# Kernel tuning notes

Hardware: AMD Instinct MI355X
Metric: run time of the kernel (lower is better)

The kernel has to match this reference:

```python
import jax, jax.numpy as jnp
import numpy as np

CH = 512
CK = CH // 8  # 64

def conv1x1(w, x):
    # w: [out, in], x: [B, in, H, W] -> [B, out, H, W]
    return jnp.einsum('oc,bchw->bohw', w, x)

def maxpool2(x):
    B, C, H, W = x.shape
    return x.reshape(B, C, H // 2, 2, W // 2, 2).max(axis=(3, 5))

def setup_inputs() -> dict:
    key = jax.random.key(0)
    ks = jax.random.split(key, 5)
    B, H, W = 16, 64, 64
    x = jax.random.normal(ks[0], (B, CH, H, W), dtype=jnp.float32)
    scale = 1.0 / np.sqrt(CH)
    Wt = jax.random.normal(ks[1], (CK, CH), dtype=jnp.float32) * scale
    Wp = jax.random.normal(ks[2], (CK, CH), dtype=jnp.float32) * scale
    Wg = jax.random.normal(ks[3], (CK, CH), dtype=jnp.float32) * scale
    Wo = jax.random.normal(ks[4], (CH, CK), dtype=jnp.float32) * (1.0 / np.sqrt(CK))
    gamma = jnp.float32(0.1)  # nonzero so backward through attention path is exercised
    return {'x': x, 'Wt': Wt, 'Wp': Wp, 'Wg': Wg, 'Wo': Wo, 'gamma': gamma}

def reference(x, Wt, Wp, Wg, Wo, gamma):
    B, C, H, W = x.shape
    N = H * W          # query positions
    M = N // 4         # pooled key/value positions
    theta = conv1x1(Wt, x).reshape(B, CK, N)            # [B, ck, N]
    phi = maxpool2(conv1x1(Wp, x)).reshape(B, CK, M)    # [B, ck, M]
    g = maxpool2(conv1x1(Wg, x)).reshape(B, CK, M)      # [B, ck, M]
    scores = jnp.einsum('bcn,bcm->bnm', theta, phi)     # [B, N, M]
    beta = jax.nn.softmax(scores, axis=-1)
    o = jnp.einsum('bcm,bnm->bcn', g, beta)             # [B, ck, N]
    o = conv1x1(Wo, o.reshape(B, CK, H, W))             # [B, C, H, W]
    return gamma * o + x
```

## Files before the change

### kernel.cpp

```cpp
#include <hip/hip_runtime.h>

#define CHN 512
#define CKD 64
#define NPOS 4096
#define MPOS 1024

typedef __attribute__((ext_vector_type(8))) short bf16x8;
typedef __attribute__((ext_vector_type(4))) float f32x4;
typedef __attribute__((ext_vector_type(8))) unsigned short u16x8;

static constexpr size_t OFF_O   = 0;
static constexpr size_t OFF_THT = 4194304;
static constexpr size_t OFF_PHT = 6291456;
static constexpr size_t OFF_GB  = 6815744;
static constexpr size_t OFF_WBF = 7340032;
static constexpr size_t OFF_WOB = 7389184;

__device__ __forceinline__ unsigned short f2bf(float f) {
  union { float f; unsigned int u; } v; v.f = f;
  unsigned int r = v.u + 0x7FFFu + ((v.u >> 16) & 1u);
  return (unsigned short)(r >> 16);
}

__device__ __forceinline__ void gl2lds16(const void* g, void* l) {
  __builtin_amdgcn_global_load_lds(
      (const __attribute__((address_space(1))) unsigned int*)g,
      (__attribute__((address_space(3))) unsigned int*)l, 16, 0, 0);
}

__global__ __launch_bounds__(256) void prep_w_kernel(
    const float* __restrict__ Wt, const float* __restrict__ Wp,
    const float* __restrict__ Wg, const float* __restrict__ Wo,
    unsigned short* __restrict__ wbf, unsigned short* __restrict__ wobf)
{
  int id = blockIdx.x * 256 + threadIdx.x;
  if (id < 98304) {
    int mat = id >> 15, r = id & 32767;
    const float* W = (mat == 0) ? Wt : (mat == 1) ? Wp : Wg;
    wbf[id] = f2bf(W[r]);
  } else {
    int j = id - 98304;
    wobf[j] = f2bf(Wo[j]);
  }
}

__global__ __launch_bounds__(256) void qkv_fused_kernel(
    const float* __restrict__ x,
    const unsigned short* __restrict__ wbf,
    unsigned short* __restrict__ thT, unsigned short* __restrict__ phT,
    unsigned short* __restrict__ gbf)
{
  __shared__ unsigned short sXb[64 * 132];
  __shared__ unsigned short sW[3 * 64 * 64];

  const int bx = blockIdx.x;
  const int b  = blockIdx.y;
  const int t  = threadIdx.x;
  const int w   = t >> 6;
  const int l   = t & 63;
  const int l16 = l & 15;
  const int lhi = l >> 4;
  const int n0  = bx * 128;

  const float* xb = x + (size_t)b * CHN * NPOS + n0;

  f32x4 acc[3][2][4];
#pragma unroll
  for (int m = 0; m < 3; ++m)
#pragma unroll
    for (int nf = 0; nf < 2; ++nf)
#pragma unroll
      for (int ckf = 0; ckf < 4; ++ckf) acc[m][nf][ckf] = (f32x4){0.f, 0.f, 0.f, 0.f};

  for (int c0 = 0; c0 < CHN; c0 += 64) {
    if (c0) __syncthreads();
#pragma unroll
    for (int i = 0; i < 8; ++i) {
      int row  = i * 8 + (t >> 5);
      int col4 = t & 31;
      float4 v = *(const float4*)(xb + (size_t)(c0 + row) * NPOS + col4 * 4);
      ushort4 u;
      u.x = f2bf(v.x); u.y = f2bf(v.y); u.z = f2bf(v.z); u.w = f2bf(v.w);
      *(ushort4*)&sXb[row * 132 + col4 * 4] = u;
    }
#pragma unroll
    for (int mi = 0; mi < 6; ++mi) {
      int mat = mi >> 1;
      int row = ((mi & 1) * 4 + w) * 8 + (l >> 3);
      int sbyte = (l & 7) * 16;
      const char* g = (const char*)wbf +
          ((((size_t)mat * 64 + row) * CHN + c0) << 1) + (sbyte ^ ((row & 7) << 4));
      gl2lds16(g, (char*)sW + mi * 4096 + w * 1024);
    }
    __syncthreads();

#pragma unroll
    for (int ks = 0; ks < 2; ++ks) {
      const int cu = ks * 32 + lhi * 8;
      bf16x8 a[2];
#pragma unroll
      for (int nf = 0; nf < 2; ++nf) {
        const int rn = 16 * w + 64 * nf + l16;
        bf16x8 av;
#pragma unroll
        for (int e = 0; e < 8; ++e)
          av[e] = (short)sXb[(cu + e) * 132 + rn];
        a[nf] = av;
      }
#pragma unroll
      for (int m = 0; m < 3; ++m)
#pragma unroll
        for (int ckf = 0; ckf < 4; ++ckf) {
          int rw = ckf * 16 + l16;
          bf16x8 bb = *(const bf16x8*)&sW[m * 4096 + rw * 64 + ((ks * 32 + lhi * 8) ^ ((rw & 7) * 8))];
          acc[m][0][ckf] = __builtin_amdgcn_mfma_f32_16x16x32_bf16(a[0], bb, acc[m][0][ckf], 0, 0, 0);
          acc[m][1][ckf] = __builtin_amdgcn_mfma_f32_16x16x32_bf16(a[1], bb, acc[m][1][ckf], 0, 0, 0);
        }
    }
  }

  unsigned short* th = thT + (size_t)b * NPOS * 64;
#pragma unroll
  for (int nf = 0; nf < 2; ++nf)
#pragma unroll
    for (int r = 0; r < 4; ++r) {
      int n = n0 + 16 * w + 64 * nf + lhi * 4 + r;
#pragma unroll
      for (int ckf = 0; ckf < 4; ++ckf)
        th[(size_t)n * 64 + ckf * 16 + l16] = f2bf(acc[0][nf][ckf][r]);
    }

  unsigned short* ph = phT + (size_t)b * MPOS * 64;
  unsigned short* gb = gbf + (size_t)b * CKD * MPOS;
#pragma unroll
  for (int pr = 0; pr < 2; ++pr) {
    int mcol = bx * 32 + 8 * w + lhi * 2 + pr;
#pragma unroll
    for (int ckf = 0; ckf < 4; ++ckf) {
      int ck = ckf * 16 + l16;
      float vp = fmaxf(fmaxf(acc[1][0][ckf][2 * pr], acc[1][0][ckf][2 * pr + 1]),
                       fmaxf(acc[1][1][ckf][2 * pr], acc[1][1][ckf][2 * pr + 1]));
      float vg = fmaxf(fmaxf(acc[2][0][ckf][2 * pr], acc[2][0][ckf][2 * pr + 1]),
                       fmaxf(acc[2][1][ckf][2 * pr], acc[2][1][ckf][2 * pr + 1]));
      ph[(size_t)mcol * 64 + ck] = f2bf(vp);
      gb[(size_t)ck * MPOS + mcol] = f2bf(vg);
    }
  }
}

__global__ __launch_bounds__(256) void attn_kernel(
    const unsigned short* __restrict__ thT,
    const unsigned short* __restrict__ phT,
    const unsigned short* __restrict__ gbf,
    unsigned short* __restrict__ obf)
{
  __shared__ unsigned short sTh[64 * 64];
  __shared__ unsigned short sPhi[64 * 64];
  __shared__ unsigned short sG[64 * 64];
  __shared__ unsigned short sP[64 * 64];

  const int qt = blockIdx.x;
  const int b  = blockIdx.y;
  const int t  = threadIdx.x;
  const int w   = t >> 6;
  const int l   = t & 63;
  const int l16 = l & 15;
  const int lhi = l >> 4;

  {
    const unsigned short* src = thT + ((size_t)b * NPOS + (size_t)qt * 64) * 64;
#pragma unroll
    for (int c = t; c < 512; c += 256) {
      int row = c >> 3, c8 = c & 7;
      *(f32x4*)&sTh[row * 64 + ((c8 * 8) ^ ((row & 7) * 8))] =
          *(const f32x4*)(src + row * 64 + c8 * 8);
    }
  }

  f32x4 oacc[4];
  float m_run[4], l_run[4];
#pragma unroll
  for (int i = 0; i < 4; ++i) {
    oacc[i] = (f32x4){0.f, 0.f, 0.f, 0.f};
    m_run[i] = -1e30f; l_run[i] = 0.f;
  }

  const unsigned short* phb = phT + (size_t)b * MPOS * 64;
  const unsigned short* gb  = gbf + (size_t)b * CKD * MPOS;

  for (int mt = 0; mt < 16; ++mt) {
    __syncthreads();
#pragma unroll
    for (int c = t; c < 512; c += 256) {
      int row = c >> 3, c8 = c & 7;
      *(f32x4*)&sPhi[row * 64 + ((c8 * 8) ^ ((row & 7) * 8))] =
          *(const f32x4*)(phb + (size_t)(mt * 64 + row) * 64 + c8 * 8);
    }
#pragma unroll
    for (int c = t; c < 512; c += 256) {
      int row = c >> 3, c8 = c & 7;
      *(f32x4*)&sG[row * 64 + ((c8 * 8) ^ ((row & 7) * 8))] =
          *(const f32x4*)(gb + (size_t)row * MPOS + mt * 64 + c8 * 8);
    }
    __syncthreads();

    f32x4 sacc[4];
#pragma unroll
    for (int mf = 0; mf < 4; ++mf) sacc[mf] = (f32x4){0.f, 0.f, 0.f, 0.f};
#pragma unroll
    for (int ks = 0; ks < 2; ++ks) {
      const int q  = 16 * w + l16;
      const int ob = lhi * 8 + 32 * ks;
      bf16x8 a = *(const bf16x8*)&sTh[q * 64 + (ob ^ ((q & 7) * 8))];
#pragma unroll
      for (int mf = 0; mf < 4; ++mf) {
        const int m = l16 + 16 * mf;
        bf16x8 bb = *(const bf16x8*)&sPhi[m * 64 + (ob ^ ((m & 7) * 8))];
        sacc[mf] = __builtin_amdgcn_mfma_f32_16x16x32_bf16(a, bb, sacc[mf], 0, 0, 0);
      }
    }

    float sc[4];
#pragma unroll
    for (int r = 0; r < 4; ++r) {
      float mx = fmaxf(fmaxf(sacc[0][r], sacc[1][r]), fmaxf(sacc[2][r], sacc[3][r]));
      mx = fmaxf(mx, __shfl_xor(mx, 1, 64));
      mx = fmaxf(mx, __shfl_xor(mx, 2, 64));
      mx = fmaxf(mx, __shfl_xor(mx, 4, 64));
      mx = fmaxf(mx, __shfl_xor(mx, 8, 64));
      float mnew = fmaxf(m_run[r], mx);
      sc[r] = __expf(m_run[r] - mnew);
      m_run[r] = mnew;
      float rs = 0.f;
#pragma unroll
      for (int mf = 0; mf < 4; ++mf) {
        float p = __expf(sacc[mf][r] - mnew);
        sacc[mf][r] = p;
        rs += p;
      }
      rs += __shfl_xor(rs, 1, 64);
      rs += __shfl_xor(rs, 2, 64);
      rs += __shfl_xor(rs, 4, 64);
      rs += __shfl_xor(rs, 8, 64);
      l_run[r] = l_run[r] * sc[r] + rs;
    }

#pragma unroll
    for (int r = 0; r < 4; ++r) {
      const int qq = 16 * w + lhi * 4 + r;
      const int swz = (qq & 7) * 8;
#pragma unroll
      for (int mf = 0; mf < 4; ++mf) {
        const int m = l16 + 16 * mf;
        sP[qq * 64 + ((m & 0x38) ^ swz) + (m & 7)] = f2bf(sacc[mf][r]);
      }
    }

#pragma unroll
    for (int ckf = 0; ckf < 4; ++ckf)
#pragma unroll
      for (int r = 0; r < 4; ++r) oacc[ckf][r] *= sc[r];

#pragma unroll
    for (int ks = 0; ks < 2; ++ks) {
      const int q  = 16 * w + l16;
      const int ob = lhi * 8 + 32 * ks;
      bf16x8 a = *(const bf16x8*)&sP[q * 64 + (ob ^ ((q & 7) * 8))];
#pragma unroll
      for (int ckf = 0; ckf < 4; ++ckf) {
        const int ck = l16 + 16 * ckf;
        bf16x8 bb = *(const bf16x8*)&sG[ck * 64 + (ob ^ ((ck & 7) * 8))];
        oacc[ckf] = __builtin_amdgcn_mfma_f32_16x16x32_bf16(a, bb, oacc[ckf], 0, 0, 0);
      }
    }
  }

  float inv[4];
#pragma unroll
  for (int r = 0; r < 4; ++r) inv[r] = 1.0f / l_run[r];

  unsigned short* ob = obf + (size_t)b * NPOS * 64;
#pragma unroll
  for (int r = 0; r < 4; ++r) {
    int n = qt * 64 + 16 * w + lhi * 4 + r;
#pragma unroll
    for (int ckf = 0; ckf < 4; ++ckf)
      ob[(size_t)n * 64 + ckf * 16 + l16] = f2bf(oacc[ckf][r] * inv[r]);
  }
}

__global__ __launch_bounds__(256) void outconv_mfma_kernel(
    const float* __restrict__ x,
    const unsigned short* __restrict__ wobf,
    const unsigned short* __restrict__ obf,
    const float* __restrict__ gamma_p, float* __restrict__ outp)
{
  __shared__ unsigned short sO[256 * 64];
  __shared__ unsigned short sWo[64 * 64];

  const int nt = blockIdx.x;
  const int ct = blockIdx.y;
  const int b  = blockIdx.z;
  const int t  = threadIdx.x;
  const int w   = t >> 6;
  const int l   = t & 63;
  const int l16 = l & 15;
  const int lhi = l >> 4;

#pragma unroll
  for (int i = 0; i < 8; ++i) {
    int cidx = i * 256 + t;
    int row = cidx >> 3, sub = cidx & 7;
    const char* g = (const char*)obf +
        ((((size_t)b * NPOS + nt * 256 + row) * 64) << 1) + ((sub * 16) ^ ((row & 7) << 4));
    gl2lds16(g, (char*)sO + (i * 256 + w * 64) * 16);
  }
#pragma unroll
  for (int i = 0; i < 2; ++i) {
    int cidx = i * 256 + t;
    int row = cidx >> 3, sub = cidx & 7;
    const char* g = (const char*)wobf +
        ((((size_t)(ct * 64 + row)) * 64) << 1) + ((sub * 16) ^ ((row & 7) << 4));
    gl2lds16(g, (char*)sWo + (i * 256 + w * 64) * 16);
  }

  const float gv = *gamma_p;
  float4 xv[4][4];
#pragma unroll
  for (int nf = 0; nf < 4; ++nf) {
    const int n = nt * 256 + w * 64 + nf * 16 + lhi * 4;
#pragma unroll
    for (int cf = 0; cf < 4; ++cf) {
      const int co = ct * 64 + cf * 16 + l16;
      xv[nf][cf] = *(const float4*)(x + ((size_t)b * CHN + co) * NPOS + n);
    }
  }
  __syncthreads();

  f32x4 acc[4][4];
#pragma unroll
  for (int nf = 0; nf < 4; ++nf)
#pragma unroll
    for (int cf = 0; cf < 4; ++cf) acc[nf][cf] = (f32x4){0.f, 0.f, 0.f, 0.f};

#pragma unroll
  for (int ks = 0; ks < 2; ++ks) {
    const int cu = ks * 32 + lhi * 8;
    bf16x8 a[4];
#pragma unroll
    for (int nf = 0; nf < 4; ++nf) {
      int rn = w * 64 + nf * 16 + l16;
      a[nf] = *(const bf16x8*)&sO[rn * 64 + (cu ^ ((rn & 7) * 8))];
    }
#pragma unroll
    for (int cf = 0; cf < 4; ++cf) {
      int rw = cf * 16 + l16;
      bf16x8 bb = *(const bf16x8*)&sWo[rw * 64 + (cu ^ ((rw & 7) * 8))];
#pragma unroll
      for (int nf = 0; nf < 4; ++nf)
        acc[nf][cf] = __builtin_amdgcn_mfma_f32_16x16x32_bf16(a[nf], bb, acc[nf][cf], 0, 0, 0);
    }
  }

#pragma unroll
  for (int nf = 0; nf < 4; ++nf) {
    const int n = nt * 256 + w * 64 + nf * 16 + lhi * 4;
#pragma unroll
    for (int cf = 0; cf < 4; ++cf) {
      const int co = ct * 64 + cf * 16 + l16;
      const size_t off = ((size_t)b * CHN + co) * NPOS + n;
      float4 rr;
      rr.x = fmaf(gv, acc[nf][cf][0], xv[nf][cf].x);
      rr.y = fmaf(gv, acc[nf][cf][1], xv[nf][cf].y);
      rr.z = fmaf(gv, acc[nf][cf][2], xv[nf][cf].z);
      rr.w = fmaf(gv, acc[nf][cf][3], xv[nf][cf].w);
      *(float4*)(outp + off) = rr;
    }
  }
}

extern "C" void kernel_launch(void* const* d_in, const int* in_sizes, int n_in,
                              void* d_out, int out_size, void* d_ws, size_t ws_size,
                              hipStream_t stream)
{
  const float* x     = (const float*)d_in[0];
  const float* Wt    = (const float*)d_in[1];
  const float* Wp    = (const float*)d_in[2];
  const float* Wg    = (const float*)d_in[3];
  const float* Wo    = (const float*)d_in[4];
  const float* gamma = (const float*)d_in[5];
  float* out = (float*)d_out;
  float* ws  = (float*)d_ws;

  unsigned short* obf = (unsigned short*)(ws + OFF_O);
  unsigned short* thT = (unsigned short*)(ws + OFF_THT);
  unsigned short* phT = (unsigned short*)(ws + OFF_PHT);
  unsigned short* gbf = (unsigned short*)(ws + OFF_GB);
  unsigned short* wbf = (unsigned short*)(ws + OFF_WBF);
  unsigned short* wob = (unsigned short*)(ws + OFF_WOB);

  prep_w_kernel<<<dim3(512), 256, 0, stream>>>(Wt, Wp, Wg, Wo, wbf, wob);
  qkv_fused_kernel<<<dim3(32, 16), 256, 0, stream>>>(x, wbf, thT, phT, gbf);
  attn_kernel<<<dim3(64, 16), 256, 0, stream>>>(thT, phT, gbf, obf);
  outconv_mfma_kernel<<<dim3(16, 8, 16), 256, 0, stream>>>(x, wob, obf, gamma, out);
}
```

Before: 141.5 us.

## Double attention query tile per block and load K/V tiles via direct global-to-LDS

The attention kernel now processes 128 query rows per block (two 16-row fragments per wave) instead of 64, so each loaded phi/g tile is reused across twice as many queries and the grid halves. Tile loads switch from register-staged copies to the gl2lds16 direct global-to-LDS path with the swizzle applied on the source address. Softmax shuffles are narrowed to 16-lane width. Costs are doubled accumulator register pressure and fewer blocks (512), which may reduce occupancy and latency hiding.

```diff
diff --git a/kernel.cpp b/kernel.cpp
--- a/kernel.cpp
+++ b/kernel.cpp
@@ -154,10 +154,10 @@
     const unsigned short* __restrict__ gbf,
     unsigned short* __restrict__ obf)
 {
-  __shared__ unsigned short sTh[64 * 64];
+  __shared__ unsigned short sTh[128 * 64];
+  __shared__ unsigned short sP [128 * 64];
   __shared__ unsigned short sPhi[64 * 64];
-  __shared__ unsigned short sG[64 * 64];
-  __shared__ unsigned short sP[64 * 64];
+  __shared__ unsigned short sG [64 * 64];
 
   const int qt = blockIdx.x;
   const int b  = blockIdx.y;
@@ -168,22 +168,25 @@
   const int lhi = l >> 4;
 
   {
-    const unsigned short* src = thT + ((size_t)b * NPOS + (size_t)qt * 64) * 64;
-#pragma unroll
-    for (int c = t; c < 512; c += 256) {
-      int row = c >> 3, c8 = c & 7;
-      *(f32x4*)&sTh[row * 64 + ((c8 * 8) ^ ((row & 7) * 8))] =
-          *(const f32x4*)(src + row * 64 + c8 * 8);
-    }
-  }
-
-  f32x4 oacc[4];
-  float m_run[4], l_run[4];
-#pragma unroll
-  for (int i = 0; i < 4; ++i) {
-    oacc[i] = (f32x4){0.f, 0.f, 0.f, 0.f};
-    m_run[i] = -1e30f; l_run[i] = 0.f;
-  }
+    const char* srcb = (const char*)(thT + ((size_t)b * NPOS + (size_t)qt * 128) * 64);
+#pragma unroll
+    for (int i = 0; i < 4; ++i) {
+      int cidx = i * 256 + t;
+      int row = cidx >> 3, sub = cidx & 7;
+      gl2lds16(srcb + row * 128 + ((sub * 16) ^ ((row & 7) << 4)),
+               (char*)sTh + (i * 256 + w * 64) * 16);
+    }
+  }
+
+  f32x4 oacc[2][4];
+  float m_run[2][4], l_run[2][4];
+#pragma unroll
+  for (int qf = 0; qf < 2; ++qf)
+#pragma unroll
+    for (int i = 0; i < 4; ++i) {
+      oacc[qf][i] = (f32x4){0.f, 0.f, 0.f, 0.f};
+      m_run[qf][i] = -1e30f; l_run[qf][i] = 0.f;
+    }
 
   const unsigned short* phb = phT + (size_t)b * MPOS * 64;
   const unsigned short* gb  = gbf + (size_t)b * CKD * MPOS;
@@ -191,101 +194,113 @@
   for (int mt = 0; mt < 16; ++mt) {
     __syncthreads();
 #pragma unroll
-    for (int c = t; c < 512; c += 256) {
-      int row = c >> 3, c8 = c & 7;
-      *(f32x4*)&sPhi[row * 64 + ((c8 * 8) ^ ((row & 7) * 8))] =
-          *(const f32x4*)(phb + (size_t)(mt * 64 + row) * 64 + c8 * 8);
-    }
-#pragma unroll
-    for (int c = t; c < 512; c += 256) {
-      int row = c >> 3, c8 = c & 7;
-      *(f32x4*)&sG[row * 64 + ((c8 * 8) ^ ((row & 7) * 8))] =
-          *(const f32x4*)(gb + (size_t)row * MPOS + mt * 64 + c8 * 8);
+    for (int i = 0; i < 2; ++i) {
+      int cidx = i * 256 + t;
+      int row = cidx >> 3, sub = cidx & 7;
+      gl2lds16((const char*)(phb + (size_t)(mt * 64 + row) * 64) +
+                   ((sub * 16) ^ ((row & 7) << 4)),
+               (char*)sPhi + (i * 256 + w * 64) * 16);
+      gl2lds16((const char*)(gb + (size_t)row * MPOS + mt * 64) +
+                   ((sub * 16) ^ ((row & 7) << 4)),
+               (char*)sG + (i * 256 + w * 64) * 16);
     }
     __syncthreads();
 
-    f32x4 sacc[4];
-#pragma unroll
-    for (int mf = 0; mf < 4; ++mf) sacc[mf] = (f32x4){0.f, 0.f, 0.f, 0.f};
-#pragma unroll
-    for (int ks = 0; ks < 2; ++ks) {
-      const int q  = 16 * w + l16;
-      const int ob = lhi * 8 + 32 * ks;
-      bf16x8 a = *(const bf16x8*)&sTh[q * 64 + (ob ^ ((q & 7) * 8))];
-#pragma unroll
-      for (int mf = 0; mf < 4; ++mf) {
-        const int m = l16 + 16 * mf;
-        bf16x8 bb = *(const bf16x8*)&sPhi[m * 64 + (ob ^ ((m & 7) * 8))];
-        sacc[mf] = __builtin_amdgcn_mfma_f32_16x16x32_bf16(a, bb, sacc[mf], 0, 0, 0);
+    f32x4 sacc[2][4];
+#pragma unroll
+    for (int qf = 0; qf < 2; ++qf)
+#pragma unroll
+      for (int mf = 0; mf < 4; ++mf) sacc[qf][mf] = (f32x4){0.f, 0.f, 0.f, 0.f};
+#pragma unroll
+    for (int qf = 0; qf < 2; ++qf)
+#pragma unroll
+      for (int ks = 0; ks < 2; ++ks) {
+        const int q  = 32 * w + 16 * qf + l16;
+        const int ob = lhi * 8 + 32 * ks;
+        bf16x8 a = *(const bf16x8*)&sTh[q * 64 + (ob ^ ((q & 7) * 8))];
+#pragma unroll
+        for (int mf = 0; mf < 4; ++mf) {
+          const int m = l16 + 16 * mf;
+          bf16x8 bb = *(const bf16x8*)&sPhi[m * 64 + (ob ^ ((m & 7) * 8))];
+          sacc[qf][mf] = __builtin_amdgcn_mfma_f32_16x16x32_bf16(a, bb, sacc[qf][mf], 0, 0, 0);
+        }
       }
-    }
-
-    float sc[4];
+
+    float sc[2][4];
+#pragma unroll
+    for (int qf = 0; qf < 2; ++qf) {
+#pragma unroll
+      for (int r = 0; r < 4; ++r) {
+        float mx = fmaxf(fmaxf(sacc[qf][0][r], sacc[qf][1][r]),
+                         fmaxf(sacc[qf][2][r], sacc[qf][3][r]));
+        mx = fmaxf(mx, __shfl_xor(mx, 1, 16));
+        mx = fmaxf(mx, __shfl_xor(mx, 2, 16));
+        mx = fmaxf(mx, __shfl_xor(mx, 4, 16));
+        mx = fmaxf(mx, __shfl_xor(mx, 8, 16));
+        float mnew = fmaxf(m_run[qf][r], mx);
+        sc[qf][r] = __expf(m_run[qf][r] - mnew);
+        m_run[qf][r] = mnew;
+        float rs = 0.f;
+#pragma unroll
+        for (int mf = 0; mf < 4; ++mf) {
+          float p = __expf(sacc[qf][mf][r] - mnew);
+          sacc[qf][mf][r] = p;
+          rs += p;
+        }
+        rs += __shfl_xor(rs, 1, 16);
+        rs += __shfl_xor(rs, 2, 16);
+        rs += __shfl_xor(rs, 4, 16);
+        rs += __shfl_xor(rs, 8, 16);
+        l_run[qf][r] = l_run[qf][r] * sc[qf][r] + rs;
+      }
+#pragma unroll
+      for (int r = 0; r < 4; ++r) {
+        const int qq = 32 * w + 16 * qf + lhi * 4 + r;
+        const int swz = (qq & 7) * 8;
+#pragma unroll
+        for (int mf = 0; mf < 4; ++mf) {
+          const int m = l16 + 16 * mf;
+          sP[qq * 64 + ((m & 0x38) ^ swz) + (m & 7)] = f2bf(sacc[qf][mf][r]);
+        }
+      }
+    }
+
+#pragma unroll
+    for (int qf = 0; qf < 2; ++qf)
+#pragma unroll
+      for (int ckf = 0; ckf < 4; ++ckf)
+#pragma unroll
+        for (int r = 0; r < 4; ++r) oacc[qf][ckf][r] *= sc[qf][r];
+
+#pragma unroll
+    for (int qf = 0; qf < 2; ++qf)
+#pragma unroll
+      for (int ks = 0; ks < 2; ++ks) {
+        const int q  = 32 * w + 16 * qf + l16;
+        const int ob = lhi * 8 + 32 * ks;
+        bf16x8 a = *(const bf16x8*)&sP[q * 64 + (ob ^ ((q & 7) * 8))];
+#pragma unroll
+        for (int ckf = 0; ckf < 4; ++ckf) {
+          const int ck = l16 + 16 * ckf;
+          bf16x8 bb = *(const bf16x8*)&sG[ck * 64 + (ob ^ ((ck & 7) * 8))];
+          oacc[qf][ckf] = __builtin_amdgcn_mfma_f32_16x16x32_bf16(a, bb, oacc[qf][ckf], 0, 0, 0);
+        }
+      }
+  }
+
+  unsigned short* ob = obf + (size_t)b * NPOS * 64;
+#pragma unroll
+  for (int qf = 0; qf < 2; ++qf) {
+    float inv[4];
+#pragma unroll
+    for (int r = 0; r < 4; ++r) inv[r] = 1.0f / l_run[qf][r];
 #pragma unroll
     for (int r = 0; r < 4; ++r) {
-      float mx = fmaxf(fmaxf(sacc[0][r], sacc[1][r]), fmaxf(sacc[2][r], sacc[3][r]));
-      mx = fmaxf(mx, __shfl_xor(mx, 1, 64));
-      mx = fmaxf(mx, __shfl_xor(mx, 2, 64));
-      mx = fmaxf(mx, __shfl_xor(mx, 4, 64));
-      mx = fmaxf(mx, __shfl_xor(mx, 8, 64));
-      float mnew = fmaxf(m_run[r], mx);
-      sc[r] = __expf(m_run[r] - mnew);
-      m_run[r] = mnew;
-      float rs = 0.f;
-#pragma unroll
-      for (int mf = 0; mf < 4; ++mf) {
-        float p = __expf(sacc[mf][r] - mnew);
-        sacc[mf][r] = p;
-        rs += p;
-      }
-      rs += __shfl_xor(rs, 1, 64);
-      rs += __shfl_xor(rs, 2, 64);
-      rs += __shfl_xor(rs, 4, 64);
-      rs += __shfl_xor(rs, 8, 64);
-      l_run[r] = l_run[r] * sc[r] + rs;
-    }
-
-#pragma unroll
-    for (int r = 0; r < 4; ++r) {
-      const int qq = 16 * w + lhi * 4 + r;
-      const int swz = (qq & 7) * 8;
-#pragma unroll
-      for (int mf = 0; mf < 4; ++mf) {
-        const int m = l16 + 16 * mf;
-        sP[qq * 64 + ((m & 0x38) ^ swz) + (m & 7)] = f2bf(sacc[mf][r]);
-      }
-    }
-
-#pragma unroll
-    for (int ckf = 0; ckf < 4; ++ckf)
-#pragma unroll
-      for (int r = 0; r < 4; ++r) oacc[ckf][r] *= sc[r];
-
-#pragma unroll
-    for (int ks = 0; ks < 2; ++ks) {
-      const int q  = 16 * w + l16;
-      const int ob = lhi * 8 + 32 * ks;
-      bf16x8 a = *(const bf16x8*)&sP[q * 64 + (ob ^ ((q & 7) * 8))];
-#pragma unroll
-      for (int ckf = 0; ckf < 4; ++ckf) {
-        const int ck = l16 + 16 * ckf;
-        bf16x8 bb = *(const bf16x8*)&sG[ck * 64 + (ob ^ ((ck & 7) * 8))];
-        oacc[ckf] = __builtin_amdgcn_mfma_f32_16x16x32_bf16(a, bb, oacc[ckf], 0, 0, 0);
-      }
-    }
-  }
-
-  float inv[4];
-#pragma unroll
-  for (int r = 0; r < 4; ++r) inv[r] = 1.0f / l_run[r];
-
-  unsigned short* ob = obf + (size_t)b * NPOS * 64;
-#pragma unroll
-  for (int r = 0; r < 4; ++r) {
-    int n = qt * 64 + 16 * w + lhi * 4 + r;
-#pragma unroll
-    for (int ckf = 0; ckf < 4; ++ckf)
-      ob[(size_t)n * 64 + ckf * 16 + l16] = f2bf(oacc[ckf][r] * inv[r]);
+      int n = qt * 128 + 32 * w + 16 * qf + lhi * 4 + r;
+#pragma unroll
+      for (int ckf = 0; ckf < 4; ++ckf)
+        ob[(size_t)n * 64 + ckf * 16 + l16] = f2bf(oacc[qf][ckf][r] * inv[r]);
+    }
   }
 }
 
@@ -401,6 +416,6 @@
 
   prep_w_kernel<<<dim3(512), 256, 0, stream>>>(Wt, Wp, Wg, Wo, wbf, wob);
   qkv_fused_kernel<<<dim3(32, 16), 256, 0, stream>>>(x, wbf, thT, phT, gbf);
-  attn_kernel<<<dim3(64, 16), 256, 0, stream>>>(thT, phT, gbf, obf);
+  attn_kernel<<<dim3(32, 16), 256, 0, stream>>>(thT, phT, gbf, obf);
   outconv_mfma_kernel<<<dim3(16, 8, 16), 256, 0, stream>>>(x, wob, obf, gamma, out);
 }
```

Result: no change. 142.1 us (+0.5%).
